# Optimization experiments

Measured on AMD Instinct MI355X. Metric: run time of the kernel, lower is better.

Reference implementation:

```python
import jax, jax.numpy as jnp
import numpy as np

L = 16384   # sequence length
H = 1024    # feature dim
P = 1024    # state dim (ssm_size=2048, conj_sym=True -> P = ssm_size//2)
STEP_RESCALE = 1.0
CLIP_MAX = -1e-4


def setup_inputs() -> dict:
    key = jax.random.key(0)
    ks = jax.random.split(key, 7)
    log_dt_min, log_dt_max = np.log(0.001), np.log(0.1)
    return {
        "input_sequence": jax.random.normal(ks[0], (L, H), jnp.float32),
        # stable eigenvalues: negative real part
        "Lambda_re": -(jnp.abs(jax.random.normal(ks[1], (P,), jnp.float32)) + 1e-3),
        "Lambda_im": jax.random.normal(ks[2], (P,), jnp.float32) * jnp.pi,
        "B": jax.random.normal(ks[3], (P, H, 2), jnp.float32) / np.sqrt(H),
        "C": jax.random.normal(ks[4], (H, P, 2), jnp.float32) / np.sqrt(P),
        "D": jax.random.normal(ks[5], (H,), jnp.float32),
        "log_step": jax.random.uniform(ks[6], (P, 1), jnp.float32,
                                        minval=log_dt_min, maxval=log_dt_max),
    }


def _binop(q_i, q_j):
    # binary operator of the linear recurrence (diagonal A)
    A_i, b_i = q_i
    A_j, b_j = q_j
    return (A_j * A_i, A_j * b_i + b_j)


def reference(input_sequence, Lambda_re, Lambda_im, B, C, D, log_step):
    # clip_eigs=True: clamp real part at -1e-4
    Lambda = jnp.minimum(Lambda_re, CLIP_MAX) + 1j * Lambda_im        # (P,) complex64
    B_tilde = B[..., 0] + 1j * B[..., 1]                              # (P, H)
    C_tilde = C[..., 0] + 1j * C[..., 1]                              # (H, P)
    step = STEP_RESCALE * jnp.exp(log_step[:, 0])                     # (P,)
    # ZOH discretisation
    Lambda_bar = jnp.exp(Lambda * step)                               # (P,)
    B_bar = ((Lambda_bar - 1.0) / Lambda)[:, None] * B_tilde          # (P, H)
    # input projection: (L,H) @ (H,P) -> (L,P) complex
    Bu = input_sequence.astype(B_bar.dtype) @ B_bar.T
    Lam = jnp.broadcast_to(Lambda_bar, Bu.shape)                      # (L, P)
    # parallel (Blelchley-style) associative scan over time
    _, xs = jax.lax.associative_scan(_binop, (Lam, Bu))               # (L, P)
    # output projection; conj_sym=True -> factor 2 on the real part
    ys = 2.0 * jnp.real(xs @ C_tilde.T)                               # (L, H)
    return ys + input_sequence * D
```

## Files before the change

### kernel.cpp

```cpp
#include <hip/hip_runtime.h>
#include <hip/hip_bf16.h>
#include <stdint.h>


#define L_SEQ 16384
#define H_DIM 1024
#define P_DIM 1024
#define NCH   256
#define TCH   64

typedef __bf16 bf16x8 __attribute__((ext_vector_type(8)));
typedef float  floatx4 __attribute__((ext_vector_type(4)));
using bf16 = __hip_bfloat16;

__device__ __forceinline__ void gld_lds16(const void* g, void* l) {
    __builtin_amdgcn_global_load_lds(
        (const __attribute__((address_space(1))) uint32_t*)g,
        (__attribute__((address_space(3))) uint32_t*)l, 16, 0, 0);
}

__device__ __forceinline__ float lo_bf(uint32_t v) { return __uint_as_float(v << 16); }
__device__ __forceinline__ float hi_bf(uint32_t v) { return __uint_as_float(v & 0xffff0000u); }
__device__ __forceinline__ uint32_t pack_bf(float r, float i) {
    bf16 rb = __float2bfloat16(r), ib = __float2bfloat16(i);
    return ((uint32_t)(*(uint16_t*)&ib) << 16) | (uint32_t)(*(uint16_t*)&rb);
}

__device__ __forceinline__ float rd(const void* p, size_t i, int f) {
    return f ? ((const float*)p)[i]
             : __bfloat162float(((const bf16*)p)[i]);
}

__device__ __forceinline__ int detect_f32(const uint16_t* u) {
    __shared__ int cnt;
    if (threadIdx.x == 0) cnt = 0;
    __syncthreads();
    int c = 0;
    #pragma unroll
    for (int i = 0; i < 8; ++i) {
        int e = (u[threadIdx.x * 8 + i] >> 7) & 0xFF;
        c += (e >= 134);
    }
    if (c) atomicAdd(&cnt, c);
    __syncthreads();
    return cnt > 32;
}

__global__ void convert_u(const void* __restrict__ uin, bf16* __restrict__ ub) {
    const int f = detect_f32((const uint16_t*)uin);
    const size_t g = (size_t)blockIdx.x * 256 + threadIdx.x;
    if (f) {
        const float4* s = (const float4*)uin + g * 2;
        float4 a = s[0], b = s[1];
        alignas(16) bf16 t[8] = {
            __float2bfloat16(a.x), __float2bfloat16(a.y),
            __float2bfloat16(a.z), __float2bfloat16(a.w),
            __float2bfloat16(b.x), __float2bfloat16(b.y),
            __float2bfloat16(b.z), __float2bfloat16(b.w)};
        ((uint4*)ub)[g] = *(const uint4*)t;
    } else {
        ((uint4*)ub)[g] = ((const uint4*)uin)[g];
    }
}

__global__ void prep_all(const void* __restrict__ u,
                         const void* __restrict__ Lre, const void* __restrict__ Lim,
                         const void* __restrict__ lstep, const void* __restrict__ B,
                         const void* __restrict__ C, const void* __restrict__ D,
                         bf16* __restrict__ W1t, bf16* __restrict__ W2t,
                         float* __restrict__ d_f,
                         float2* __restrict__ lam, float2* __restrict__ lamT) {
    const int f = detect_f32((const uint16_t*)u);
    const int p = blockIdx.x;
    float lr = fminf(rd(Lre, p, f), -1e-4f);
    float li = rd(Lim, p, f);
    float s  = expf(rd(lstep, p, f));
    float ea = expf(lr * s);
    float lbr = ea * cosf(li * s), lbi = ea * sinf(li * s);
    float dr = lbr - 1.0f, di = lbi;
    float den = lr * lr + li * li;
    float cr = (dr * lr + di * li) / den;
    float ci = (di * lr - dr * li) / den;
    if (threadIdx.x == 0) {
        lam[p] = make_float2(lbr, lbi);
        float tr = lbr, ti = lbi;
        #pragma unroll
        for (int q = 0; q < 6; ++q) {
            float nr = tr * tr - ti * ti, ni = 2.0f * tr * ti;
            tr = nr; ti = ni;
        }
        lamT[p] = make_float2(tr, ti);
        d_f[p] = rd(D, p, f);
    }
    for (int h = threadIdx.x; h < H_DIM; h += blockDim.x) {
        size_t base = ((size_t)p * H_DIM + h) * 2;
        float br = rd(B, base + 0, f);
        float bi = rd(B, base + 1, f);
        W1t[(size_t)(2 * p)     * H_DIM + h] = __float2bfloat16(cr * br - ci * bi);
        W1t[(size_t)(2 * p + 1) * H_DIM + h] = __float2bfloat16(cr * bi + ci * br);
    }
    const int h = blockIdx.x;
    for (int q = threadIdx.x; q < P_DIM; q += blockDim.x) {
        size_t base = ((size_t)h * P_DIM + q) * 2;
        W2t[(size_t)h * (2 * P_DIM) + 2 * q]     = __float2bfloat16( 2.0f * rd(C, base + 0, f));
        W2t[(size_t)h * (2 * P_DIM) + 2 * q + 1] = __float2bfloat16(-2.0f * rd(C, base + 1, f));
    }
}


#define STAGE(b, t) do {                                                      \
    const int k0_ = (t) * 64;                                                 \
    _Pragma("unroll")                                                         \
    for (int q_ = 0; q_ < 4; ++q_) {                                          \
        const int row_ = q_ * 64 + srow;                                      \
        const int g_   = sg ^ (row_ & 7);                                     \
        gld_lds16(A  + (size_t)(bm + row_) * K + k0_ + g_ * 8,                \
                  sA + (b) * 32768 + q_ * 8192 + wave * 1024);                \
        gld_lds16(Bt + (size_t)(bn + row_) * K + k0_ + g_ * 8,                \
                  sB + (b) * 32768 + q_ * 8192 + wave * 1024);                \
    } } while (0)

#define LDA(b, mh) do {                                                       \
    _Pragma("unroll")                                                         \
    for (int mi_ = 0; mi_ < 4; ++mi_) {                                       \
        const int row_ = wm + ((mh) * 4 + mi_) * 16 + fr;                     \
        _Pragma("unroll")                                                     \
        for (int ks_ = 0; ks_ < 2; ++ks_) {                                   \
            const int ch_ = (ks_ * 4 + kq) ^ (row_ & 7);                      \
            af[mi_][ks_] = *(const bf16x8*)(sA + (b) * 32768 + row_ * 128 + ch_ * 16); \
        } } } while (0)

#define LDB(b, nh) do {                                                       \
    _Pragma("unroll")                                                         \
    for (int ni_ = 0; ni_ < 2; ++ni_) {                                       \
        const int row_ = wn + ((nh) * 2 + ni_) * 16 + fr;                     \
        _Pragma("unroll")                                                     \
        for (int ks_ = 0; ks_ < 2; ++ks_) {                                   \
            const int ch_ = (ks_ * 4 + kq) ^ (row_ & 7);                      \
            bfr[ni_][ks_] = *(const bf16x8*)(sB + (b) * 32768 + row_ * 128 + ch_ * 16); \
        } } } while (0)

#define MMA(mh, nh) do {                                                      \
    asm volatile("s_waitcnt lgkmcnt(0)" ::: "memory");                        \
    __builtin_amdgcn_sched_barrier(0);                                        \
    __builtin_amdgcn_s_setprio(1);                                            \
    _Pragma("unroll")                                                         \
    for (int mi_ = 0; mi_ < 4; ++mi_)                                         \
        _Pragma("unroll")                                                     \
        for (int ni_ = 0; ni_ < 2; ++ni_)                                     \
            _Pragma("unroll")                                                 \
            for (int ks_ = 0; ks_ < 2; ++ks_)                                 \
                acc[(mh) * 4 + mi_][(nh) * 2 + ni_] =                         \
                    __builtin_amdgcn_mfma_f32_16x16x32_bf16(                  \
                        af[mi_][ks_], bfr[ni_][ks_],                          \
                        acc[(mh) * 4 + mi_][(nh) * 2 + ni_], 0, 0, 0);        \
    __builtin_amdgcn_s_setprio(0);                                            \
} while (0)

template <int N, int K, int MODE>
__global__ __launch_bounds__(512, 2) void gemm256(
    const bf16* __restrict__ A, const bf16* __restrict__ Bt,
    bf16* __restrict__ OutBF, float* __restrict__ OutF,
    const bf16* __restrict__ U, const float* __restrict__ Dvec,
    const float2* __restrict__ lam, float2* __restrict__ aggp) {
    constexpr int NXB = N / 256;
    constexpr int KT  = K / 64;
    __shared__ alignas(16) uint8_t sA[2 * 32768];
    __shared__ alignas(16) uint8_t sB[2 * 32768];

    const int tid  = threadIdx.x;
    const int wave = tid >> 6;
    const int lane = tid & 63;
    const int bid  = blockIdx.x;
    const int xr   = bid & 7;
    const int jj   = bid >> 3;
    const int bx   = jj % NXB;
    const int by   = (jj / NXB) * 8 + xr;
    const int bm   = by * 256, bn = bx * 256;
    const int wm   = (wave >> 2) * 128, wn = (wave & 3) * 64;

    floatx4 acc[8][4] = {};

    const int fr   = lane & 15;
    const int kq   = lane >> 4;
    const int srow = tid >> 3;
    const int sg   = tid & 7;

    STAGE(0, 0);
    STAGE(1, 1);
    asm volatile("s_waitcnt vmcnt(8)" ::: "memory");
    __builtin_amdgcn_sched_barrier(0);
    __builtin_amdgcn_s_barrier();

    bf16x8 af[4][2], bfr[2][2];

    #pragma unroll 2
    for (int t = 0; t < KT; ++t) {
        const int cur = t & 1;
        LDA(cur, 0); LDB(cur, 0);
        __builtin_amdgcn_s_barrier();
        MMA(0, 0);
        LDB(cur, 1);
        __builtin_amdgcn_s_barrier();
        MMA(0, 1);
        LDA(cur, 1);
        __builtin_amdgcn_s_barrier();
        MMA(1, 1);
        LDB(cur, 0);
        __builtin_amdgcn_s_barrier();
        MMA(1, 0);
        __builtin_amdgcn_s_barrier();
        if (t + 2 < KT) {
            STAGE(cur, t + 2);
            asm volatile("s_waitcnt vmcnt(8)" ::: "memory");
        } else {
            asm volatile("s_waitcnt vmcnt(0)" ::: "memory");
        }
        __builtin_amdgcn_sched_barrier(0);
        __builtin_amdgcn_s_barrier();
    }

    const int col0  = bn + wn + fr;
    const int rbase = bm + wm + kq * 4;
    #pragma unroll
    for (int mi = 0; mi < 8; ++mi) {
        #pragma unroll
        for (int rr = 0; rr < 4; ++rr) {
            const int row = rbase + mi * 16 + rr;
            #pragma unroll
            for (int ni = 0; ni < 4; ++ni) {
                const int c = col0 + ni * 16;
                float v = acc[mi][ni][rr];
                if (MODE == 2) {
                    float uu = __bfloat162float(U[(size_t)row * H_DIM + c]);
                    __builtin_nontemporal_store(v + uu * Dvec[c],
                                                &OutF[(size_t)row * N + c]);
                } else {
                    OutBF[(size_t)row * N + c] = __float2bfloat16(v);
                }
            }
        }
    }

    if (MODE == 1) {
        const int par = fr & 1;
        const int cg0 = (bm + wm) >> 6;
        #pragma unroll
        for (int ni = 0; ni < 4; ++ni) {
            const int ql = (wn + ni * 16 + (fr & ~1)) >> 1;
            const float2 lb = lam[(bn >> 1) + ql];
            const float l1r = lb.x, l1i = lb.y;
            const float l2r = l1r * l1r - l1i * l1i, l2i = 2.f * l1r * l1i;
            const float l4r = l2r * l2r - l2i * l2i, l4i = 2.f * l2r * l2i;
            const float l8r = l4r * l4r - l4i * l4i, l8i = 2.f * l4r * l4i;
            const float l12r = l8r * l4r - l8i * l4i;
            const float l12i = l8r * l4i + l8i * l4r;
            #pragma unroll
            for (int h = 0; h < 2; ++h) {
                float wr_, wi_;
                if      (kq == 0) { wr_ = l12r; wi_ = l12i; }
                else if (kq == 1) { wr_ = l8r;  wi_ = l8i;  }
                else if (kq == 2) { wr_ = l4r;  wi_ = l4i;  }
                else              { wr_ = 1.f;  wi_ = 0.f;  }
                float s = 0.f;
                #pragma unroll
                for (int mi2 = 3; mi2 >= 0; --mi2) {
                    #pragma unroll
                    for (int rr = 3; rr >= 0; --rr) {
                        float own  = acc[h * 4 + mi2][ni][rr];
                        float part = __shfl_xor(own, 1);
                        s += wr_ * own + (par ? wi_ : -wi_) * part;
                        float nr = wr_ * l1r - wi_ * l1i;
                        float nI = wr_ * l1i + wi_ * l1r;
                        wr_ = nr; wi_ = nI;
                    }
                    float nr = wr_ * l12r - wi_ * l12i;
                    float nI = wr_ * l12i + wi_ * l12r;
                    wr_ = nr; wi_ = nI;
                }
                s += __shfl_xor(s, 16);
                s += __shfl_xor(s, 32);
                float other = __shfl_xor(s, 1);
                if (kq == 0 && par == 0)
                    aggp[(size_t)(cg0 + h) * P_DIM + (bn >> 1) + ql] =
                        make_float2(s, other);
            }
        }
    }
}

__global__ void scan_phase2p(const float2* __restrict__ agg,
                             const float2* __restrict__ lamT,
                             float2* __restrict__ carry) {
    const int w = threadIdx.x >> 6;
    const int j = threadIdx.x & 63;
    const int p = blockIdx.x * 4 + w;
    const float2 A = lamT[p];
    float b2r = A.x * A.x - A.y * A.y, b2i = 2.f * A.x * A.y;
    float Br = b2r * b2r - b2i * b2i, Bi = 2.f * b2r * b2i;
    float2 a[4];
    #pragma unroll
    for (int k = 0; k < 4; ++k) a[k] = agg[(size_t)(4 * j + k) * P_DIM + p];
    float xr = 0.f, xi = 0.f;
    #pragma unroll
    for (int k = 0; k < 4; ++k) {
        float nr = A.x * xr - A.y * xi + a[k].x;
        float ni = A.x * xi + A.y * xr + a[k].y;
        xr = nr; xi = ni;
    }
    float cr = Br, ci = Bi, vr = xr, vi = xi;
    #pragma unroll
    for (int d = 1; d < 64; d <<= 1) {
        float pvr = __shfl_up(vr, d), pvi = __shfl_up(vi, d);
        float pcr = __shfl_up(cr, d), pci = __shfl_up(ci, d);
        if (j >= d) {
            float nvr = cr * pvr - ci * pvi + vr;
            float nvi = cr * pvi + ci * pvr + vi;
            float ncr = cr * pcr - ci * pci;
            float nci = cr * pci + ci * pcr;
            vr = nvr; vi = nvi; cr = ncr; ci = nci;
        }
    }
    float sr = __shfl_up(vr, 1), si = __shfl_up(vi, 1);
    if (j == 0) { sr = 0.f; si = 0.f; }
    #pragma unroll
    for (int k = 0; k < 4; ++k) {
        carry[(size_t)(4 * j + k) * P_DIM + p] = make_float2(sr, si);
        float nr = A.x * sr - A.y * si + a[k].x;
        float ni = A.x * si + A.y * sr + a[k].y;
        sr = nr; si = ni;
    }
}

__global__ void scan_phase3(uint32_t* __restrict__ BuX,
                            const float2* __restrict__ lam,
                            const float2* __restrict__ carry) {
    const int p = blockIdx.y * 256 + threadIdx.x;
    const int c = blockIdx.x;
    const float2 lb = lam[p];
    const float2 c0 = carry[(size_t)c * P_DIM + p];
    float xr = c0.x, xi = c0.y;
    uint32_t* b = BuX + (size_t)c * TCH * P_DIM + p;
    #pragma unroll 4
    for (int j = 0; j < TCH; ++j) {
        uint32_t v = *b;
        float nr = lb.x * xr - lb.y * xi + lo_bf(v);
        float ni = lb.x * xi + lb.y * xr + hi_bf(v);
        xr = nr; xi = ni;
        *b = pack_bf(xr, xi);
        b += P_DIM;
    }
}

extern "C" void kernel_launch(void* const* d_in, const int* in_sizes, int n_in,
                              void* d_out, int out_size, void* d_ws, size_t ws_size,
                              hipStream_t stream) {
    float* out = (float*)d_out;

    char* w = (char*)d_ws;
    w += 256;
    float2* lam   = (float2*)w;  w += (size_t)P_DIM * 8;
    float2* lamT  = (float2*)w;  w += (size_t)P_DIM * 8;
    float*  d_f   = (float*)w;   w += (size_t)H_DIM * 4;
    float2* agg   = (float2*)w;  w += (size_t)NCH * P_DIM * 8;
    float2* carry = (float2*)w;  w += (size_t)NCH * P_DIM * 8;
    bf16*   W1t   = (bf16*)w;    w += (size_t)2 * P_DIM * H_DIM * 2;
    bf16*   W2t   = (bf16*)w;    w += (size_t)H_DIM * 2 * P_DIM * 2;
    bf16*   ub    = (bf16*)w;    w += (size_t)L_SEQ * H_DIM * 2;
    bf16*   Xbuf  = (bf16*)w;

    convert_u<<<(L_SEQ * H_DIM / 8) / 256, 256, 0, stream>>>(d_in[0], ub);
    prep_all<<<P_DIM, 256, 0, stream>>>(d_in[0], d_in[1], d_in[2], d_in[6],
                                        d_in[3], d_in[4], d_in[5],
                                        W1t, W2t, d_f, lam, lamT);

    gemm256<2 * P_DIM, H_DIM, 1><<<(2 * P_DIM / 256) * (L_SEQ / 256), 512, 0, stream>>>(
        ub, W1t, Xbuf, nullptr, nullptr, nullptr, lam, agg);

    scan_phase2p<<<P_DIM / 4, 256, 0, stream>>>(agg, lamT, carry);
    scan_phase3<<<dim3(NCH, P_DIM / 256), 256, 0, stream>>>(
        (uint32_t*)Xbuf, lam, carry);

    gemm256<H_DIM, 2 * P_DIM, 2><<<(H_DIM / 256) * (L_SEQ / 256), 512, 0, stream>>>(
        Xbuf, W2t, nullptr, out, ub, d_f, nullptr, nullptr);
}
```

Before: 332.8 us.

## Issue all LDS fragment loads up front and overlap with MFMA via partial lgkmcnt waits

The GEMM inner loop now loads every A and B fragment for the k-tile into separate register sets up front. It then runs the MFMA quadrants under staged lgkmcnt waits, so later LDS reads overlap earlier matrix math. The four intra-iteration workgroup barriers between quadrants are removed, and B fragments are no longer reloaded. This raises register pressure with launch_bounds(512,2), which risks spills. The lgkmcnt counts must match the issued loads exactly.

```diff
diff --git a/kernel.cpp b/kernel.cpp
--- a/kernel.cpp
+++ b/kernel.cpp
@@ -108,6 +108,8 @@
 }
 
 
+#define SB0 __builtin_amdgcn_sched_barrier(0)
+
 #define STAGE(b, t) do {                                                      \
     const int k0_ = (t) * 64;                                                 \
     _Pragma("unroll")                                                         \
@@ -120,30 +122,27 @@
                   sB + (b) * 32768 + q_ * 8192 + wave * 1024);                \
     } } while (0)
 
-#define LDA(b, mh) do {                                                       \
+#define LDF_A(dst, b, mh) do {                                                \
     _Pragma("unroll")                                                         \
     for (int mi_ = 0; mi_ < 4; ++mi_) {                                       \
         const int row_ = wm + ((mh) * 4 + mi_) * 16 + fr;                     \
         _Pragma("unroll")                                                     \
         for (int ks_ = 0; ks_ < 2; ++ks_) {                                   \
             const int ch_ = (ks_ * 4 + kq) ^ (row_ & 7);                      \
-            af[mi_][ks_] = *(const bf16x8*)(sA + (b) * 32768 + row_ * 128 + ch_ * 16); \
+            dst[mi_][ks_] = *(const bf16x8*)(sA + (b) * 32768 + row_ * 128 + ch_ * 16); \
         } } } while (0)
 
-#define LDB(b, nh) do {                                                       \
+#define LDF_B(dst, b, nh) do {                                                \
     _Pragma("unroll")                                                         \
     for (int ni_ = 0; ni_ < 2; ++ni_) {                                       \
         const int row_ = wn + ((nh) * 2 + ni_) * 16 + fr;                     \
         _Pragma("unroll")                                                     \
         for (int ks_ = 0; ks_ < 2; ++ks_) {                                   \
             const int ch_ = (ks_ * 4 + kq) ^ (row_ & 7);                      \
-            bfr[ni_][ks_] = *(const bf16x8*)(sB + (b) * 32768 + row_ * 128 + ch_ * 16); \
+            dst[ni_][ks_] = *(const bf16x8*)(sB + (b) * 32768 + row_ * 128 + ch_ * 16); \
         } } } while (0)
 
-#define MMA(mh, nh) do {                                                      \
-    asm volatile("s_waitcnt lgkmcnt(0)" ::: "memory");                        \
-    __builtin_amdgcn_sched_barrier(0);                                        \
-    __builtin_amdgcn_s_setprio(1);                                            \
+#define MMA(afv, bfv, mh, nh) do {                                            \
     _Pragma("unroll")                                                         \
     for (int mi_ = 0; mi_ < 4; ++mi_)                                         \
         _Pragma("unroll")                                                     \
@@ -152,9 +151,8 @@
             for (int ks_ = 0; ks_ < 2; ++ks_)                                 \
                 acc[(mh) * 4 + mi_][(nh) * 2 + ni_] =                         \
                     __builtin_amdgcn_mfma_f32_16x16x32_bf16(                  \
-                        af[mi_][ks_], bfr[ni_][ks_],                          \
+                        afv[mi_][ks_], bfv[ni_][ks_],                         \
                         acc[(mh) * 4 + mi_][(nh) * 2 + ni_], 0, 0, 0);        \
-    __builtin_amdgcn_s_setprio(0);                                            \
 } while (0)
 
 template <int N, int K, int MODE>
@@ -189,26 +187,34 @@
     STAGE(0, 0);
     STAGE(1, 1);
     asm volatile("s_waitcnt vmcnt(8)" ::: "memory");
-    __builtin_amdgcn_sched_barrier(0);
+    SB0;
     __builtin_amdgcn_s_barrier();
 
-    bf16x8 af[4][2], bfr[2][2];
+    bf16x8 afA[4][2], afB[4][2], bf0[2][2], bf1[2][2];
 
     #pragma unroll 2
     for (int t = 0; t < KT; ++t) {
         const int cur = t & 1;
-        LDA(cur, 0); LDB(cur, 0);
-        __builtin_amdgcn_s_barrier();
-        MMA(0, 0);
-        LDB(cur, 1);
-        __builtin_amdgcn_s_barrier();
-        MMA(0, 1);
-        LDA(cur, 1);
-        __builtin_amdgcn_s_barrier();
-        MMA(1, 1);
-        LDB(cur, 0);
-        __builtin_amdgcn_s_barrier();
-        MMA(1, 0);
+        LDF_A(afA, cur, 0); SB0;
+        LDF_B(bf0, cur, 0); SB0;
+        LDF_B(bf1, cur, 1); SB0;
+        LDF_A(afB, cur, 1); SB0;
+        asm volatile("s_waitcnt lgkmcnt(12)" ::: "memory");
+        SB0;
+        __builtin_amdgcn_s_setprio(1);
+        MMA(afA, bf0, 0, 0);
+        __builtin_amdgcn_s_setprio(0);
+        asm volatile("s_waitcnt lgkmcnt(8)" ::: "memory");
+        SB0;
+        __builtin_amdgcn_s_setprio(1);
+        MMA(afA, bf1, 0, 1);
+        __builtin_amdgcn_s_setprio(0);
+        asm volatile("s_waitcnt lgkmcnt(0)" ::: "memory");
+        SB0;
+        __builtin_amdgcn_s_setprio(1);
+        MMA(afB, bf0, 1, 0);
+        MMA(afB, bf1, 1, 1);
+        __builtin_amdgcn_s_setprio(0);
         __builtin_amdgcn_s_barrier();
         if (t + 2 < KT) {
             STAGE(cur, t + 2);
@@ -216,7 +222,7 @@
         } else {
             asm volatile("s_waitcnt vmcnt(0)" ::: "memory");
         }
-        __builtin_amdgcn_sched_barrier(0);
+        SB0;
         __builtin_amdgcn_s_barrier();
     }
 
```

New measurement: 408.5 us. +22.8%, slower.
